# Kernel tuning notes

Hardware: AMD Instinct MI355X
Metric: run time of the kernel (lower is better)

## Reference

```python
import jax, jax.numpy as jnp
import numpy as np
from jax import lax

B, C, L, H = 32, 256, 1280, 5
D = L // H  # head dim = 256
EPS = 1e-5


def setup_inputs() -> dict:
    key = jax.random.key(0)
    ks = jax.random.split(key, 16)
    s = 0.02
    inp = {
        "x": jax.random.normal(ks[0], (B, C, L), jnp.float32),
        # rank encoder Linear(L, L)
        "re_w": jax.random.normal(ks[1], (L, L), jnp.float32) * s,
        "re_b": jnp.zeros((L,), jnp.float32),
        # layer norms
        "ln1_g": jnp.ones((L,), jnp.float32), "ln1_b": jnp.zeros((L,), jnp.float32),
        "ln2_g": jnp.ones((L,), jnp.float32), "ln2_b": jnp.zeros((L,), jnp.float32),
        # attention projections (stored [in, out]; y @ W + b)
        "wq": jax.random.normal(ks[2], (L, L), jnp.float32) * s, "bq": jnp.zeros((L,), jnp.float32),
        "wk": jax.random.normal(ks[3], (L, L), jnp.float32) * s, "bk": jnp.zeros((L,), jnp.float32),
        "wv": jax.random.normal(ks[4], (L, L), jnp.float32) * s, "bv": jnp.zeros((L,), jnp.float32),
        "wo": jax.random.normal(ks[5], (L, L), jnp.float32) * s, "bo": jnp.zeros((L,), jnp.float32),
        # FFN (ffn_size == hidden_size == L in this module)
        "ffn_w1": jax.random.normal(ks[6], (L, L), jnp.float32) * s, "ffn_b1": jnp.zeros((L,), jnp.float32),
        "ffn_w2": jax.random.normal(ks[7], (L, L), jnp.float32) * s, "ffn_b2": jnp.zeros((L,), jnp.float32),
        # Conv1d(C, C, k=3, stride=1, pad=1, bias=False) + BatchNorm1d (eval) + ReLU
        "conv_w": jax.random.normal(ks[8], (C, C, 3), jnp.float32) * (2.0 / (C * 3)) ** 0.5,
        "bn_g": jnp.ones((C,), jnp.float32), "bn_b": jnp.zeros((C,), jnp.float32),
        "bn_m": jnp.zeros((C,), jnp.float32), "bn_v": jnp.ones((C,), jnp.float32),
    }
    return inp


def _layernorm(t, g, b):
    m = jnp.mean(t, axis=-1, keepdims=True)
    v = jnp.var(t, axis=-1, keepdims=True)
    return (t - m) * lax.rsqrt(v + EPS) * g + b


def reference(x, re_w, re_b, ln1_g, ln1_b, ln2_g, ln2_b,
              wq, bq, wk, bk, wv, bv, wo, bo,
              ffn_w1, ffn_b1, ffn_w2, ffn_b2,
              conv_w, bn_g, bn_b, bn_m, bn_v):
    b_, c_, l_ = x.shape
    # _getrank_: rank from double argsort (descending), mapped to (L - rank)/L
    rank_i = jnp.argsort(jnp.argsort(-x, axis=-1), axis=-1)
    rank = (l_ - rank_i).astype(x.dtype) / l_
    node = x + rank @ re_w + re_b                      # [B, C, L]

    # EncoderLayer: pre-LN MHSA (attn_bias is None in this call path)
    y = _layernorm(node, ln1_g, ln1_b)
    scale = D ** -0.5
    q = (y @ wq + bq).reshape(b_, c_, H, D).transpose(0, 2, 1, 3) * scale  # [B,H,C,D]
    k = (y @ wk + bk).reshape(b_, c_, H, D).transpose(0, 2, 1, 3)
    v = (y @ wv + bv).reshape(b_, c_, H, D).transpose(0, 2, 1, 3)
    attn = jax.nn.softmax(jnp.einsum('bhqd,bhkd->bhqk', q, k), axis=-1)   # [B,H,C,C]
    o = jnp.einsum('bhqk,bhkd->bhqd', attn, v)
    o = o.transpose(0, 2, 1, 3).reshape(b_, c_, l_) @ wo + bo
    h = node + o  # dropout is identity in eval

    # FFN sublayer
    y2 = _layernorm(h, ln2_g, ln2_b)
    f = jax.nn.gelu(y2 @ ffn_w1 + ffn_b1, approximate=False) @ ffn_w2 + ffn_b2
    h = h + f                                           # [B, C, L]

    # ConvBNRelu: Conv1d(k=3, s=1, p=1, no bias) -> BN (eval stats) -> ReLU
    conv = lax.conv_general_dilated(h, conv_w, window_strides=(1,),
                                    padding=[(1, 1)],
                                    dimension_numbers=('NCH', 'OIH', 'NCH'))
    bn = (conv - bn_m[None, :, None]) * lax.rsqrt(bn_v[None, :, None] + EPS)
    bn = bn * bn_g[None, :, None] + bn_b[None, :, None]
    return jax.nn.relu(bn)
```

## Files before the change

### kernel.cpp

```cpp
#include <hip/hip_runtime.h>
#include <hip/hip_bf16.h>
#include <stdint.h>

#define L_   1280
#define B_   32
#define C_   256
#define H_   5
#define D_   256
#define BC_  8192
#define EPSV 1e-5f

typedef __attribute__((ext_vector_type(8))) short bf16x8;
typedef __attribute__((ext_vector_type(4))) float f32x4;
typedef __hip_bfloat16 bf16;

__device__ __forceinline__ bf16 f2bf(float v) { return __float2bfloat16(v); }

#define GLDS16(gptr, lptr)                                                        \
    __builtin_amdgcn_global_load_lds(                                             \
        (const __attribute__((address_space(1))) void*)(gptr),                    \
        (__attribute__((address_space(3))) void*)(lptr), 16, 0, 0)

struct WtArgs { const float* src[7]; bf16* dst[7]; };

__global__ __launch_bounds__(256) void transpose7(WtArgs a) {
    const int mat = blockIdx.z;
    const float* src = a.src[mat];
    bf16* dst = a.dst[mat];
    __shared__ float tile[32][33];
    const int bx = blockIdx.x * 32;
    const int by = blockIdx.y * 32;
    const int tx = threadIdx.x, ty = threadIdx.y;
    #pragma unroll
    for (int r = ty; r < 32; r += 8)
        tile[r][tx] = src[(size_t)(by + r) * L_ + bx + tx];
    __syncthreads();
    #pragma unroll
    for (int r = ty; r < 32; r += 8)
        dst[(size_t)(bx + r) * L_ + by + tx] = f2bf(tile[tx][r]);
}

__global__ __launch_bounds__(256) void prep_conv(const float* cw, const float* g, const float* b,
                                                 const float* m, const float* v,
                                                 bf16* WT, float* sc, float* bi) {
    const int i = blockIdx.x * 256 + threadIdx.x;
    if (i < 3 * 256 * 256) {
        const int co = i / 768;
        const int r = i - co * 768;
        const int t = r >> 8, ci = r & 255;
        WT[i] = f2bf(cw[(co * 256 + ci) * 3 + t]);
    }
    if (i < 256) {
        const float s = g[i] * rsqrtf(v[i] + EPSV);
        sc[i] = s;
        bi[i] = b[i] - m[i] * s;
    }
}

__global__ __launch_bounds__(256) void rank_kernel(const float* __restrict__ x, bf16* __restrict__ R) {
    __shared__ float vals[L_];
    __shared__ float sv[L_];
    __shared__ int hist[256];
    __shared__ int pfx[256];
    __shared__ int cur[256];
    const int row = blockIdx.x, tid = threadIdx.x;
    const float* src = x + (size_t)row * L_;
    for (int i = tid; i < L_; i += 256) vals[i] = src[i];
    hist[tid] = 0;
    __syncthreads();
    float myv[5]; int myb[5];
    #pragma unroll
    for (int ii = 0; ii < 5; ii++) {
        const float v = vals[tid + ii * 256];
        int bk = (int)((4.0f - v) * 32.0f);
        bk = bk < 0 ? 0 : (bk > 255 ? 255 : bk);
        myv[ii] = v; myb[ii] = bk;
        atomicAdd(&hist[bk], 1);
    }
    __syncthreads();
    pfx[tid] = hist[tid];
    __syncthreads();
    for (int off = 1; off < 256; off <<= 1) {
        int t = (tid >= off) ? pfx[tid - off] : 0;
        __syncthreads();
        pfx[tid] += t;
        __syncthreads();
    }
    cur[tid] = pfx[tid] - hist[tid];
    __syncthreads();
    #pragma unroll
    for (int ii = 0; ii < 5; ii++) {
        const int pos = atomicAdd(&cur[myb[ii]], 1);
        sv[pos] = myv[ii];
    }
    __syncthreads();
    #pragma unroll
    for (int ii = 0; ii < 5; ii++) {
        const int bk = myb[ii]; const float v = myv[ii];
        const int s = pfx[bk] - hist[bk], e = pfx[bk];
        int cg = s;
        for (int p = s; p < e; p++) cg += (sv[p] > v) ? 1 : 0;
        R[(size_t)row * L_ + tid + ii * 256] = f2bf((float)(L_ - cg) * (1.0f / L_));
    }
}

__global__ __launch_bounds__(256) void ln_kernel(const float* __restrict__ in,
                                                 const float* __restrict__ g,
                                                 const float* __restrict__ b,
                                                 bf16* __restrict__ out) {
    const int row = blockIdx.x, tid = threadIdx.x;
    const float* src = in + (size_t)row * L_;
    float4 va = ((const float4*)src)[tid];
    float s = va.x + va.y + va.z + va.w;
    float ss = va.x * va.x + va.y * va.y + va.z * va.z + va.w * va.w;
    float4 vb = {0, 0, 0, 0};
    if (tid < 64) {
        vb = ((const float4*)src)[256 + tid];
        s += vb.x + vb.y + vb.z + vb.w;
        ss += vb.x * vb.x + vb.y * vb.y + vb.z * vb.z + vb.w * vb.w;
    }
    #pragma unroll
    for (int off = 32; off > 0; off >>= 1) {
        s += __shfl_down(s, off, 64);
        ss += __shfl_down(ss, off, 64);
    }
    __shared__ float rs[4], rss[4];
    __shared__ float mean_s, rstd_s;
    if ((tid & 63) == 0) { rs[tid >> 6] = s; rss[tid >> 6] = ss; }
    __syncthreads();
    if (tid == 0) {
        const float S = rs[0] + rs[1] + rs[2] + rs[3];
        const float SS = rss[0] + rss[1] + rss[2] + rss[3];
        const float m = S * (1.0f / L_);
        const float var = SS * (1.0f / L_) - m * m;
        mean_s = m; rstd_s = rsqrtf(var + EPSV);
    }
    __syncthreads();
    const float m = mean_s, r = rstd_s;
    {
        const int c = tid * 4;
        bf16 t4[4];
        t4[0] = f2bf((va.x - m) * r * g[c + 0] + b[c + 0]);
        t4[1] = f2bf((va.y - m) * r * g[c + 1] + b[c + 1]);
        t4[2] = f2bf((va.z - m) * r * g[c + 2] + b[c + 2]);
        t4[3] = f2bf((va.w - m) * r * g[c + 3] + b[c + 3]);
        *(uint2*)(out + (size_t)row * L_ + c) = *(uint2*)t4;
    }
    if (tid < 64) {
        const int c = 1024 + tid * 4;
        bf16 t4[4];
        t4[0] = f2bf((vb.x - m) * r * g[c + 0] + b[c + 0]);
        t4[1] = f2bf((vb.y - m) * r * g[c + 1] + b[c + 1]);
        t4[2] = f2bf((vb.z - m) * r * g[c + 2] + b[c + 2]);
        t4[3] = f2bf((vb.w - m) * r * g[c + 3] + b[c + 3]);
        *(uint2*)(out + (size_t)row * L_ + c) = *(uint2*)t4;
    }
}

__global__ __launch_bounds__(256) void softmax_kernel(const float* __restrict__ S, bf16* __restrict__ P) {
    const int row = blockIdx.x * 4 + (threadIdx.x >> 6);
    const int l = threadIdx.x & 63;
    const float4 v = *(const float4*)(S + (size_t)row * 256 + l * 4);
    float mx = fmaxf(fmaxf(v.x, v.y), fmaxf(v.z, v.w));
    #pragma unroll
    for (int off = 1; off < 64; off <<= 1) mx = fmaxf(mx, __shfl_xor(mx, off, 64));
    const float e0 = expf(v.x - mx), e1 = expf(v.y - mx), e2 = expf(v.z - mx), e3 = expf(v.w - mx);
    float sm = e0 + e1 + e2 + e3;
    #pragma unroll
    for (int off = 1; off < 64; off <<= 1) sm += __shfl_xor(sm, off, 64);
    const float inv = 1.0f / sm;
    bf16 t4[4] = { f2bf(e0 * inv), f2bf(e1 * inv), f2bf(e2 * inv), f2bf(e3 * inv) };
    *(uint2*)(P + (size_t)row * 256 + l * 4) = *(uint2*)t4;
}

__global__ __launch_bounds__(256) void zero_pads(bf16* h2T) {
    const int i = blockIdx.x * 256 + threadIdx.x;
    const int b = i >> 9;
    const int which = (i >> 8) & 1;
    const int ci = i & 255;
    const long row = which ? 1281 : 0;
    h2T[(long)b * (1282 * 256) + row * 256 + ci] = f2bf(0.0f);
}

struct GemmP {
    const bf16* A;  long lda, sA1, sA2;
    const bf16* Bt; long ldb, sB1, sB2;
    int zmod;
    int K;
    float* outF; bf16* outB; bf16* outB2; long ldc, sC1, sC2;
    const float* bias; const float* bias2;
    const float* res; long ldres, sR1, sR2;
    const float* rowscale; const float* rowbias;
    float scale;
};

constexpr int E_F32_BIAS_RES = 0;
constexpr int E_VT = 3;
constexpr int E_F32 = 4;
constexpr int E_BF16 = 5;
constexpr int E_GELU = 6;
constexpr int E_FFN2T = 7;
constexpr int E_CONVBNR = 8;
constexpr int E_QK = 9;

template <int EPI>
__global__ __launch_bounds__(256) void gemm_bt(GemmP p) {
    const int nwg  = gridDim.x * gridDim.y * gridDim.z;
    const int orig = (blockIdx.z * gridDim.y + blockIdx.y) * gridDim.x + blockIdx.x;
    const int qq = nwg >> 3, rr = nwg & 7;
    const int xcd = orig & 7, pos = orig >> 3;
    const int wgid = (xcd < rr ? xcd * (qq + 1) : rr * (qq + 1) + (xcd - rr) * qq) + pos;
    const int bx = wgid % gridDim.x;
    const int t1 = wgid / gridDim.x;
    const int by = t1 % gridDim.y;
    const int bz = t1 / gridDim.y;

    const int zq = bz / p.zmod, zr = bz % p.zmod;
    const bf16* A  = p.A  + (long)zq * p.sA1 + (long)zr * p.sA2;
    const bf16* Bt = p.Bt + (long)zq * p.sB1 + (long)zr * p.sB2;
    const int row0 = by * 128, col0 = bx * 128;

    __shared__ __align__(16) bf16 ldsA[2][128 * 32];
    __shared__ __align__(16) bf16 ldsB[2][128 * 32];

    const int tid = threadIdx.x;
    const int l = tid & 63, w = tid >> 6;
    const int wr = w >> 1, wc = w & 1;

    f32x4 acc[4][4];
    #pragma unroll
    for (int m = 0; m < 4; m++)
        #pragma unroll
        for (int n = 0; n < 4; n++)
            acc[m][n] = (f32x4){0.f, 0.f, 0.f, 0.f};

    const bf16* gA = A  + (long)(row0 + w * 16 + (l >> 2)) * p.lda + (l & 3) * 8;
    const bf16* gB = Bt + (long)(col0 + w * 16 + (l >> 2)) * p.ldb + (l & 3) * 8;
    const long aStep = 64 * p.lda, bStep = 64 * p.ldb;

    auto STAGE = [&](int buf) {
        GLDS16(gA,         &ldsA[buf][w * 512]);
        GLDS16(gA + aStep, &ldsA[buf][2048 + w * 512]);
        GLDS16(gB,         &ldsB[buf][w * 512]);
        GLDS16(gB + bStep, &ldsB[buf][2048 + w * 512]);
        gA += 32; gB += 32;
    };
    auto COMPUTE = [&](int buf) {
        bf16x8 aF[4], bF[4];
        #pragma unroll
        for (int m = 0; m < 4; m++)
            aF[m] = *(const bf16x8*)(&ldsA[buf][(wr * 64 + m * 16 + (l & 15)) * 32 + (l >> 4) * 8]);
        #pragma unroll
        for (int n = 0; n < 4; n++)
            bF[n] = *(const bf16x8*)(&ldsB[buf][(wc * 64 + n * 16 + (l & 15)) * 32 + (l >> 4) * 8]);
        #pragma unroll
        for (int m = 0; m < 4; m++)
            #pragma unroll
            for (int n = 0; n < 4; n++)
                acc[m][n] = __builtin_amdgcn_mfma_f32_16x16x32_bf16(aF[m], bF[n], acc[m][n], 0, 0, 0);
    };

    const int nt = p.K >> 5;
    STAGE(0);
    __syncthreads();
    int cur = 0;
    for (int t = 0; t < nt - 1; ++t) {
        STAGE(cur ^ 1);
        COMPUTE(cur);
        __syncthreads();
        cur ^= 1;
    }
    COMPUTE(cur);

    const long cz = (long)zq * p.sC1 + (long)zr * p.sC2;
    const long rz = (long)zq * p.sR1 + (long)zr * p.sR2;
    #pragma unroll
    for (int m = 0; m < 4; m++) {
        #pragma unroll
        for (int n = 0; n < 4; n++) {
            const int gcol = col0 + wc * 64 + n * 16 + (l & 15);
            #pragma unroll
            for (int j = 0; j < 4; j++) {
                const int grow = row0 + wr * 64 + m * 16 + (l >> 4) * 4 + j;
                const float v = acc[m][n][j];
                if constexpr (EPI == E_F32_BIAS_RES) {
                    p.outF[cz + (long)grow * p.ldc + gcol] =
                        v + p.bias[gcol] + p.res[rz + (long)grow * p.ldres + gcol];
                } else if constexpr (EPI == E_VT) {
                    const int b_ = grow >> 8, c_ = grow & 255;
                    const int h_ = gcol >> 8, d_ = gcol & 255;
                    p.outB[(((long)(b_ * H_ + h_) * 256 + d_) << 8) + c_] = f2bf(v + p.bias[gcol]);
                } else if constexpr (EPI == E_F32) {
                    p.outF[cz + (long)grow * p.ldc + gcol] = v;
                } else if constexpr (EPI == E_BF16) {
                    p.outB[cz + (long)grow * p.ldc + gcol] = f2bf(v);
                } else if constexpr (EPI == E_GELU) {
                    const float t = v + p.bias[gcol];
                    p.outB[cz + (long)grow * p.ldc + gcol] =
                        f2bf(0.5f * t * (1.0f + erff(t * 0.70710678f)));
                } else if constexpr (EPI == E_FFN2T) {
                    const float t = v + p.bias[gcol] + p.res[rz + (long)grow * p.ldres + gcol];
                    const int b_ = grow >> 8, ci = grow & 255;
                    p.outB[(long)b_ * (1282 * 256) + (long)(gcol + 1) * 256 + ci] = f2bf(t);
                } else if constexpr (EPI == E_CONVBNR) {
                    const float t = v * p.rowscale[grow] + p.rowbias[grow];
                    p.outF[cz + (long)grow * p.ldc + gcol] = fmaxf(t, 0.0f);
                } else if constexpr (EPI == E_QK) {
                    if (gcol < 1280) {
                        p.outB[(long)grow * L_ + gcol] = f2bf((v + p.bias[gcol]) * p.scale);
                    } else {
                        const int c2 = gcol - 1280;
                        p.outB2[(long)grow * L_ + c2] = f2bf(v + p.bias2[c2]);
                    }
                }
            }
        }
    }
}

extern "C" void kernel_launch(void* const* d_in, const int* in_sizes, int n_in,
                              void* d_out, int out_size, void* d_ws, size_t ws_size,
                              hipStream_t stream) {
    const float* x    = (const float*)d_in[0];
    const float* re_w = (const float*)d_in[1];
    const float* re_b = (const float*)d_in[2];
    const float* ln1g = (const float*)d_in[3];
    const float* ln1b = (const float*)d_in[4];
    const float* ln2g = (const float*)d_in[5];
    const float* ln2b = (const float*)d_in[6];
    const float* wq   = (const float*)d_in[7];
    const float* bq   = (const float*)d_in[8];
    const float* wk   = (const float*)d_in[9];
    const float* bk   = (const float*)d_in[10];
    const float* wv   = (const float*)d_in[11];
    const float* bv   = (const float*)d_in[12];
    const float* wo   = (const float*)d_in[13];
    const float* bo   = (const float*)d_in[14];
    const float* fw1  = (const float*)d_in[15];
    const float* fb1  = (const float*)d_in[16];
    const float* fw2  = (const float*)d_in[17];
    const float* fb2  = (const float*)d_in[18];
    const float* convw = (const float*)d_in[19];
    const float* bng  = (const float*)d_in[20];
    const float* bnb  = (const float*)d_in[21];
    const float* bnm  = (const float*)d_in[22];
    const float* bnv  = (const float*)d_in[23];
    float* out = (float*)d_out;

    char* ws = (char*)d_ws;
    const size_t SZ_WT     = (size_t)L_ * L_ * 2;
    const size_t SZ_ACT_BF = (size_t)BC_ * L_ * 2;
    const size_t SZ_ACT_F  = (size_t)BC_ * L_ * 4;
    const size_t SZ_H2T    = (size_t)B_ * 1282 * 256 * 2;
    const size_t SZ_S      = (size_t)160 * 256 * 256 * 4;

    size_t off = 0;
    bf16* Wt[7];
    for (int i = 0; i < 7; i++) { Wt[i] = (bf16*)(ws + off); off += SZ_WT; }
    bf16* WconvT   = (bf16*)(ws + off); off += 393216;
    float* bnscale = (float*)(ws + off); off += 1024;
    float* bnbias  = (float*)(ws + off); off += 1024;
    bf16* RP  = (bf16*)(ws + off); off += SZ_ACT_BF;
    bf16* Yb  = (bf16*)(ws + off); off += SZ_ACT_BF;
    bf16* Qb  = (bf16*)(ws + off); off += SZ_ACT_BF;
    bf16* Kb  = (bf16*)(ws + off); off += SZ_H2T;
    float* Sb = (float*)(ws + off); off += SZ_S;
    float* node = (float*)(ws + off); off += SZ_ACT_F;
    bf16* VT = (bf16*)Sb;
    (void)in_sizes; (void)n_in; (void)out_size;

    if (ws_size < off) return;

    WtArgs wa;
    wa.src[0] = re_w; wa.src[1] = wq; wa.src[2] = wk; wa.src[3] = wv;
    wa.src[4] = wo;  wa.src[5] = fw1; wa.src[6] = fw2;
    for (int i = 0; i < 7; i++) wa.dst[i] = Wt[i];
    transpose7<<<dim3(40, 40, 7), dim3(32, 8), 0, stream>>>(wa);
    prep_conv<<<dim3(768), 256, 0, stream>>>(convw, bng, bnb, bnm, bnv, WconvT, bnscale, bnbias);

    rank_kernel<<<dim3(BC_), 256, 0, stream>>>(x, RP);

    const dim3 gBig(L_ / 128, BC_ / 128, 1);
    const dim3 gQK(2560 / 128, BC_ / 128, 1);
    const dim3 gAttn(2, 2, 160);
    const dim3 blk(256);

    {
        GemmP p{}; p.zmod = 1; p.K = L_;
        p.A = RP; p.lda = L_; p.Bt = Wt[0]; p.ldb = L_;
        p.outF = node; p.ldc = L_; p.bias = re_b; p.res = x; p.ldres = L_;
        gemm_bt<E_F32_BIAS_RES><<<gBig, blk, 0, stream>>>(p);
    }
    ln_kernel<<<dim3(BC_), blk, 0, stream>>>(node, ln1g, ln1b, Yb);
    {
        GemmP p{}; p.zmod = 1; p.K = L_;
        p.A = Yb; p.lda = L_; p.Bt = Wt[1]; p.ldb = L_;
        p.outB = Qb; p.outB2 = Kb; p.bias = bq; p.bias2 = bk; p.scale = 0.0625f;
        gemm_bt<E_QK><<<gQK, blk, 0, stream>>>(p);
    }
    {
        GemmP p{}; p.zmod = H_; p.K = 256;
        p.A = Qb;  p.lda = L_; p.sA1 = (long)C_ * L_; p.sA2 = 256;
        p.Bt = Kb; p.ldb = L_; p.sB1 = (long)C_ * L_; p.sB2 = 256;
        p.outF = Sb; p.ldc = 256; p.sC1 = (long)H_ * 65536; p.sC2 = 65536;
        gemm_bt<E_F32><<<gAttn, blk, 0, stream>>>(p);
    }
    softmax_kernel<<<dim3(160 * 256 / 4), blk, 0, stream>>>(Sb, RP);
    {
        GemmP p{}; p.zmod = 1; p.K = L_;
        p.A = Yb; p.lda = L_; p.Bt = Wt[3]; p.ldb = L_;
        p.outB = VT; p.bias = bv;
        gemm_bt<E_VT><<<gBig, blk, 0, stream>>>(p);
    }
    {
        GemmP p{}; p.zmod = H_; p.K = 256;
        p.A = RP;  p.lda = 256; p.sA1 = (long)H_ * 65536; p.sA2 = 65536;
        p.Bt = VT; p.ldb = 256; p.sB1 = (long)H_ * 65536; p.sB2 = 65536;
        p.outB = Qb; p.ldc = L_; p.sC1 = (long)C_ * L_; p.sC2 = 256;
        gemm_bt<E_BF16><<<gAttn, blk, 0, stream>>>(p);
    }
    {
        GemmP p{}; p.zmod = 1; p.K = L_;
        p.A = Qb; p.lda = L_; p.Bt = Wt[4]; p.ldb = L_;
        p.outF = node; p.ldc = L_; p.bias = bo; p.res = node; p.ldres = L_;
        gemm_bt<E_F32_BIAS_RES><<<gBig, blk, 0, stream>>>(p);
    }
    ln_kernel<<<dim3(BC_), blk, 0, stream>>>(node, ln2g, ln2b, RP);
    {
        GemmP p{}; p.zmod = 1; p.K = L_;
        p.A = RP; p.lda = L_; p.Bt = Wt[5]; p.ldb = L_;
        p.outB = Yb; p.ldc = L_; p.bias = fb1;
        gemm_bt<E_GELU><<<gBig, blk, 0, stream>>>(p);
    }
    zero_pads<<<dim3(64), blk, 0, stream>>>(Kb);
    {
        GemmP p{}; p.zmod = 1; p.K = L_;
        p.A = Yb; p.lda = L_; p.Bt = Wt[6]; p.ldb = L_;
        p.outB = Kb; p.bias = fb2; p.res = node; p.ldres = L_;
        gemm_bt<E_FFN2T><<<gBig, blk, 0, stream>>>(p);
    }
    {
        GemmP p{}; p.zmod = 1; p.K = 768;
        p.A = WconvT; p.lda = 768;
        p.Bt = Kb; p.ldb = 256; p.sB1 = 1282 * 256;
        p.outF = out; p.ldc = L_; p.sC1 = (long)C_ * L_;
        p.rowscale = bnscale; p.rowbias = bnbias;
        gemm_bt<E_CONVBNR><<<dim3(L_ / 128, 2, B_), blk, 0, stream>>>(p);
    }
}
```

Measured before the change: 587.2 us.

## Fuse V projection into QK GEMM, store scores in bf16, relax pipeline barriers

The separate V projection GEMM is folded into the Q/K GEMM, so one launch covers 3840 output columns and reads the LayerNorm output once. The attention score matrix is now written as bf16 rather than fp32, which halves score traffic into the softmax at the cost of score precision. The GEMM main loop replaces __syncthreads with an explicit partial vmcnt wait plus s_barrier, so the next tile's loads can stay in flight during compute. This relies on the wait count matching the number of issued global-to-LDS loads per stage, and it needs Wt[1..3] to be contiguous, which the workspace layout provides.

```diff
diff --git a/kernel.cpp b/kernel.cpp
--- a/kernel.cpp
+++ b/kernel.cpp
@@ -157,14 +157,18 @@
     }
 }
 
-__global__ __launch_bounds__(256) void softmax_kernel(const float* __restrict__ S, bf16* __restrict__ P) {
+__global__ __launch_bounds__(256) void softmax_kernel(const bf16* __restrict__ S, bf16* __restrict__ P) {
     const int row = blockIdx.x * 4 + (threadIdx.x >> 6);
     const int l = threadIdx.x & 63;
-    const float4 v = *(const float4*)(S + (size_t)row * 256 + l * 4);
-    float mx = fmaxf(fmaxf(v.x, v.y), fmaxf(v.z, v.w));
+    const bf16* src = S + (size_t)row * 256 + l * 4;
+    uint2 raw = *(const uint2*)src;
+    bf16 s4[4]; *(uint2*)s4 = raw;
+    float v0 = __bfloat162float(s4[0]), v1 = __bfloat162float(s4[1]);
+    float v2 = __bfloat162float(s4[2]), v3 = __bfloat162float(s4[3]);
+    float mx = fmaxf(fmaxf(v0, v1), fmaxf(v2, v3));
     #pragma unroll
     for (int off = 1; off < 64; off <<= 1) mx = fmaxf(mx, __shfl_xor(mx, off, 64));
-    const float e0 = expf(v.x - mx), e1 = expf(v.y - mx), e2 = expf(v.z - mx), e3 = expf(v.w - mx);
+    const float e0 = expf(v0 - mx), e1 = expf(v1 - mx), e2 = expf(v2 - mx), e3 = expf(v3 - mx);
     float sm = e0 + e1 + e2 + e3;
     #pragma unroll
     for (int off = 1; off < 64; off <<= 1) sm += __shfl_xor(sm, off, 64);
@@ -187,21 +191,20 @@
     const bf16* Bt; long ldb, sB1, sB2;
     int zmod;
     int K;
-    float* outF; bf16* outB; bf16* outB2; long ldc, sC1, sC2;
-    const float* bias; const float* bias2;
+    float* outF; bf16* outB; bf16* outB2; bf16* outB3; long ldc, sC1, sC2;
+    const float* bias; const float* bias2; const float* bias3;
     const float* res; long ldres, sR1, sR2;
     const float* rowscale; const float* rowbias;
     float scale;
 };
 
 constexpr int E_F32_BIAS_RES = 0;
-constexpr int E_VT = 3;
 constexpr int E_F32 = 4;
 constexpr int E_BF16 = 5;
 constexpr int E_GELU = 6;
 constexpr int E_FFN2T = 7;
 constexpr int E_CONVBNR = 8;
-constexpr int E_QK = 9;
+constexpr int E_QKV = 9;
 
 template <int EPI>
 __global__ __launch_bounds__(256) void gemm_bt(GemmP p) {
@@ -262,14 +265,20 @@
 
     const int nt = p.K >> 5;
     STAGE(0);
-    __syncthreads();
     int cur = 0;
     for (int t = 0; t < nt - 1; ++t) {
         STAGE(cur ^ 1);
+        asm volatile("s_waitcnt vmcnt(4)" ::: "memory");
+        __builtin_amdgcn_sched_barrier(0);
+        __builtin_amdgcn_s_barrier();
         COMPUTE(cur);
-        __syncthreads();
+        __builtin_amdgcn_sched_barrier(0);
+        __builtin_amdgcn_s_barrier();
         cur ^= 1;
     }
+    asm volatile("s_waitcnt vmcnt(0)" ::: "memory");
+    __builtin_amdgcn_sched_barrier(0);
+    __builtin_amdgcn_s_barrier();
     COMPUTE(cur);
 
     const long cz = (long)zq * p.sC1 + (long)zr * p.sC2;
@@ -286,10 +295,6 @@
                 if constexpr (EPI == E_F32_BIAS_RES) {
                     p.outF[cz + (long)grow * p.ldc + gcol] =
                         v + p.bias[gcol] + p.res[rz + (long)grow * p.ldres + gcol];
-                } else if constexpr (EPI == E_VT) {
-                    const int b_ = grow >> 8, c_ = grow & 255;
-                    const int h_ = gcol >> 8, d_ = gcol & 255;
-                    p.outB[(((long)(b_ * H_ + h_) * 256 + d_) << 8) + c_] = f2bf(v + p.bias[gcol]);
                 } else if constexpr (EPI == E_F32) {
                     p.outF[cz + (long)grow * p.ldc + gcol] = v;
                 } else if constexpr (EPI == E_BF16) {
@@ -305,12 +310,18 @@
                 } else if constexpr (EPI == E_CONVBNR) {
                     const float t = v * p.rowscale[grow] + p.rowbias[grow];
                     p.outF[cz + (long)grow * p.ldc + gcol] = fmaxf(t, 0.0f);
-                } else if constexpr (EPI == E_QK) {
+                } else if constexpr (EPI == E_QKV) {
                     if (gcol < 1280) {
                         p.outB[(long)grow * L_ + gcol] = f2bf((v + p.bias[gcol]) * p.scale);
-                    } else {
+                    } else if (gcol < 2560) {
                         const int c2 = gcol - 1280;
                         p.outB2[(long)grow * L_ + c2] = f2bf(v + p.bias2[c2]);
+                    } else {
+                        const int c3 = gcol - 2560;
+                        const int b_ = grow >> 8, c_ = grow & 255;
+                        const int h_ = c3 >> 8, d_ = c3 & 255;
+                        p.outB3[(((long)(b_ * H_ + h_) * 256 + d_) << 8) + c_] =
+                            f2bf(v + p.bias3[c3]);
                     }
                 }
             }
@@ -366,7 +377,8 @@
     bf16* Kb  = (bf16*)(ws + off); off += SZ_H2T;
     float* Sb = (float*)(ws + off); off += SZ_S;
     float* node = (float*)(ws + off); off += SZ_ACT_F;
-    bf16* VT = (bf16*)Sb;
+    bf16* Sbf = (bf16*)Sb;
+    bf16* VT  = Sbf + (size_t)160 * 65536;
     (void)in_sizes; (void)n_in; (void)out_size;
 
     if (ws_size < off) return;
@@ -381,7 +393,7 @@
     rank_kernel<<<dim3(BC_), 256, 0, stream>>>(x, RP);
 
     const dim3 gBig(L_ / 128, BC_ / 128, 1);
-    const dim3 gQK(2560 / 128, BC_ / 128, 1);
+    const dim3 gQKV(3840 / 128, BC_ / 128, 1);
     const dim3 gAttn(2, 2, 160);
     const dim3 blk(256);
 
@@ -395,23 +407,18 @@
     {
         GemmP p{}; p.zmod = 1; p.K = L_;
         p.A = Yb; p.lda = L_; p.Bt = Wt[1]; p.ldb = L_;
-        p.outB = Qb; p.outB2 = Kb; p.bias = bq; p.bias2 = bk; p.scale = 0.0625f;
-        gemm_bt<E_QK><<<gQK, blk, 0, stream>>>(p);
+        p.outB = Qb; p.outB2 = Kb; p.outB3 = VT;
+        p.bias = bq; p.bias2 = bk; p.bias3 = bv; p.scale = 0.0625f;
+        gemm_bt<E_QKV><<<gQKV, blk, 0, stream>>>(p);
     }
     {
         GemmP p{}; p.zmod = H_; p.K = 256;
         p.A = Qb;  p.lda = L_; p.sA1 = (long)C_ * L_; p.sA2 = 256;
         p.Bt = Kb; p.ldb = L_; p.sB1 = (long)C_ * L_; p.sB2 = 256;
-        p.outF = Sb; p.ldc = 256; p.sC1 = (long)H_ * 65536; p.sC2 = 65536;
-        gemm_bt<E_F32><<<gAttn, blk, 0, stream>>>(p);
-    }
-    softmax_kernel<<<dim3(160 * 256 / 4), blk, 0, stream>>>(Sb, RP);
-    {
-        GemmP p{}; p.zmod = 1; p.K = L_;
-        p.A = Yb; p.lda = L_; p.Bt = Wt[3]; p.ldb = L_;
-        p.outB = VT; p.bias = bv;
-        gemm_bt<E_VT><<<gBig, blk, 0, stream>>>(p);
-    }
+        p.outB = Sbf; p.ldc = 256; p.sC1 = (long)H_ * 65536; p.sC2 = 65536;
+        gemm_bt<E_BF16><<<gAttn, blk, 0, stream>>>(p);
+    }
+    softmax_kernel<<<dim3(160 * 256 / 4), blk, 0, stream>>>(Sbf, RP);
     {
         GemmP p{}; p.zmod = H_; p.K = 256;
         p.A = RP;  p.lda = 256; p.sA1 = (long)H_ * 65536; p.sA2 = 65536;
```

Result: faster. 554.2 us (-5.6%).
